# Kernel tuning notes

Hardware: AMD Instinct MI355X
Metric: run time of the kernel (lower is better)

Reference implementation:

```python
import jax, jax.numpy as jnp
import numpy as np

H = 8
D_MODEL = 1024
D_K = D_MODEL // H
NEG = -1000000000.0


def layer_norm(x, a, b, eps=1e-06):
    # torch std: unbiased (ddof=1); module divides by (std + eps)
    mean = jnp.mean(x, axis=-1, keepdims=True)
    var = jnp.sum((x - mean) ** 2, axis=-1, keepdims=True) / (x.shape[-1] - 1)
    std = jnp.sqrt(var)
    return a * (x - mean) / (std + eps) + b


def setup_inputs() -> dict:
    key = jax.random.key(0)
    ks = jax.random.split(key, 12)
    B, S, D = 8, 1024, D_MODEL
    inp = {
        "query": jax.random.normal(ks[0], (B, S, D), jnp.float32),
        "value": jax.random.normal(ks[1], (B, S, D), jnp.float32),
        "key": jax.random.normal(ks[2], (B, S, D), jnp.float32),
        "mask": jax.random.randint(ks[3], (B, S), 0, 2, jnp.int32),
        "ln_a": jnp.ones((D,), jnp.float32),
        "ln_b": jnp.zeros((D,), jnp.float32),
        "wq": jax.random.normal(ks[4], (D, D), jnp.float32) * 0.02,
        "bq": jnp.zeros((D,), jnp.float32),
        "wk": jax.random.normal(ks[5], (D, D), jnp.float32) * 0.02,
        "bk": jnp.zeros((D,), jnp.float32),
        "wv": jax.random.normal(ks[6], (D, D), jnp.float32) * 0.02,
        "bv": jnp.zeros((D,), jnp.float32),
        "w_aoa": jax.random.normal(ks[7], (2 * D, 2 * D), jnp.float32) * 0.02,  # [out, in]
        "b_aoa": jnp.zeros((2 * D,), jnp.float32),
    }
    return inp


def reference(query, value, key, mask, ln_a, ln_b, wq, bq, wk, bk, wv, bv, w_aoa, b_aoa):
    B, S, D = query.shape
    # mask [B,S] -> [B,1,1,S]
    m = mask[:, None, None, :]
    # norm_q
    q = layer_norm(query, ln_a, ln_b)
    # QKV projections, split heads -> [B,H,S,Dk]
    def split_heads(x):
        return x.reshape(B, -1, H, D_K).transpose(0, 2, 1, 3)
    q_ = split_heads(q @ wq.T + bq)
    k_ = split_heads(key @ wk.T + bk)
    v_ = split_heads(value @ wv.T + bv)
    scores = jnp.einsum("bhqd,bhkd->bhqk", q_, k_) / jnp.sqrt(jnp.float32(D_K))
    scores = jnp.where(m == 0, NEG, scores)
    p = jax.nn.softmax(scores, axis=-1)
    x = jnp.einsum("bhqk,bhkd->bhqd", p, v_)
    x = x.transpose(0, 2, 1, 3).reshape(B, S, D)
    # AoA: concat with (normed) query, linear to 2D, GLU
    z = jnp.concatenate([x, q], axis=-1) @ w_aoa.T + b_aoa
    a, g = jnp.split(z, 2, axis=-1)
    return a * jax.nn.sigmoid(g)
```

## Files before the change

### kernel.cpp

```cpp
#include <hip/hip_runtime.h>

typedef __attribute__((ext_vector_type(8))) __bf16 bf16x8;
typedef __attribute__((ext_vector_type(4))) float f32x4;
typedef __attribute__((ext_vector_type(16))) float f32x16;
typedef __attribute__((ext_vector_type(2))) int i32x2;

__device__ __forceinline__ ushort f2b(float f) {
    uint u = __builtin_bit_cast(uint, f);
    u += 0x7fffu + ((u >> 16) & 1u);
    return (ushort)(u >> 16);
}
__device__ __forceinline__ float b2f(ushort h) {
    uint u = ((uint)h) << 16;
    return __builtin_bit_cast(float, u);
}
__device__ __forceinline__ uint cvtpk(float a, float b) {
    uint r;
    asm("v_cvt_pk_bf16_f32 %0, %1, %2" : "=v"(r) : "v"(a), "v"(b));
    return r;
}

__global__ __launch_bounds__(256) void cast_all(const float* __restrict__ key,
                                                const float* __restrict__ value,
                                                const float* __restrict__ wq,
                                                const float* __restrict__ wk,
                                                const float* __restrict__ wv,
                                                const float* __restrict__ waoa,
                                                ushort* __restrict__ keyb,
                                                ushort* __restrict__ wqb,
                                                ushort* __restrict__ wab) {
    int bid = blockIdx.x;
    int tid = threadIdx.x;
    if (bid < 16384) {
        const float* src = (bid < 8192) ? key : value;
        float4 v = *(const float4*)(src + ((size_t)(bid & 8191) * 256 + tid) * 4);
        ushort4 o;
        o.x = f2b(v.x); o.y = f2b(v.y); o.z = f2b(v.z); o.w = f2b(v.w);
        *(ushort4*)(keyb + (size_t)bid * 1024 + tid * 4) = o;
    } else if (bid < 19456) {
        int b2 = bid - 16384;
        const float* src = (b2 < 1024) ? wq : ((b2 < 2048) ? wk : wv);
        float4 v = *(const float4*)(src + ((size_t)(b2 & 1023) * 256 + tid) * 4);
        ushort4 o;
        o.x = f2b(v.x); o.y = f2b(v.y); o.z = f2b(v.z); o.w = f2b(v.w);
        *(ushort4*)(wqb + (size_t)b2 * 1024 + tid * 4) = o;
    } else {
        int b3 = bid - 19456;
        int n1 = b3 >> 1;
        int c = (b3 & 1) * 1024 + tid * 4;
        int q = ((n1 & 63) | ((n1 >> 7) << 6)) + ((n1 >> 6) & 1) * 1024;
        float4 v = *(const float4*)(waoa + (size_t)q * 2048 + c);
        ushort4 o;
        o.x = f2b(v.x); o.y = f2b(v.y); o.z = f2b(v.z); o.w = f2b(v.w);
        *(ushort4*)(wab + (size_t)n1 * 2048 + c) = o;
    }
}

__global__ __launch_bounds__(256) void ln_kernel(const float* __restrict__ x,
                                                 const float* __restrict__ ga,
                                                 const float* __restrict__ be,
                                                 ushort* __restrict__ xq) {
    const int row = blockIdx.x, tid = threadIdx.x;
    __shared__ float red[4];
    float4 v = ((const float4*)(x + (size_t)row * 1024))[tid];
    float sm = v.x + v.y + v.z + v.w;
    for (int off = 32; off; off >>= 1) sm += __shfl_xor(sm, off);
    if ((tid & 63) == 0) red[tid >> 6] = sm;
    __syncthreads();
    float mean = (red[0] + red[1] + red[2] + red[3]) * (1.f / 1024.f);
    __syncthreads();
    float dx = v.x - mean, dy = v.y - mean, dz = v.z - mean, dw = v.w - mean;
    float s2 = dx * dx + dy * dy + dz * dz + dw * dw;
    for (int off = 32; off; off >>= 1) s2 += __shfl_xor(s2, off);
    if ((tid & 63) == 0) red[tid >> 6] = s2;
    __syncthreads();
    float var = (red[0] + red[1] + red[2] + red[3]) * (1.f / 1023.f);
    float inv = 1.f / (sqrtf(var) + 1e-6f);
    float4 g = ((const float4*)ga)[tid];
    float4 bb = ((const float4*)be)[tid];
    ushort4 o;
    o.x = f2b(g.x * dx * inv + bb.x);
    o.y = f2b(g.y * dy * inv + bb.y);
    o.z = f2b(g.z * dz * inv + bb.z);
    o.w = f2b(g.w * dw * inv + bb.w);
    *(ushort4*)&xq[(size_t)row * 2048 + 1024 + tid * 4] = o;
}

template <int MODE>
__global__ __launch_bounds__(512, 2) void gemm6(const ushort* __restrict__ Aq, int ldaq,
                                                const ushort* __restrict__ B, int ldb,
                                                const float* __restrict__ bias0,
                                                void* __restrict__ out0,
                                                int K, int NB) {
    __shared__ ushort lds[2][32768];

    const int tid = threadIdx.x;
    const int w = tid >> 6, l = tid & 63;
    const int wr = w >> 2, wcn = w & 3;
    const int r16 = l & 15, g4 = l >> 4;

    const int bid = blockIdx.x;
    const int cpx = gridDim.x >> 3;
    const int swz = (bid & 7) * cpx + (bid >> 3);
    const int m0 = (swz / NB) * 256;
    const int n0 = (swz % NB) * 256;

    const ushort* A = Aq;
    const int lda = ldaq;

    const int srow8 = l >> 3;
    const int sxor8 = ((l & 7) ^ srow8) * 8;
    const ushort* As0 = A + (size_t)(m0 + w * 8 + srow8) * lda + sxor8;
    const ushort* Bs0 = B + (size_t)(n0 + w * 8 + srow8) * ldb + sxor8;

    f32x4 acc[8][4];
#pragma unroll
    for (int i = 0; i < 8; i++)
#pragma unroll
        for (int j = 0; j < 4; j++) acc[i][j] = (f32x4){0.f, 0.f, 0.f, 0.f};

    const int sw16 = (r16 & 7) << 4;
    char* ldsb = (char*)&lds[0][0];

#define STAGE_H(sel_, HS_, kt_)                                                            \
    do {                                                                                   \
        const int mat_ = (HS_)&1, half_ = (HS_) >> 1;                                      \
        const ushort* sb_ = mat_ ? Bs0 : As0;                                              \
        const int ld_ = mat_ ? ldb : lda;                                                  \
        _Pragma("unroll") for (int li_ = 0; li_ < 2; li_++) {                              \
            const ushort* src_ = sb_ + (size_t)(half_ * 128 + li_ * 64) * ld_ + (kt_)*64;  \
            int dst_ = (sel_)*65536 + mat_ * 32768 + half_ * 16384 + li_ * 8192 + w * 1024;\
            __builtin_amdgcn_global_load_lds(                                              \
                (const __attribute__((address_space(1))) void*)src_,                       \
                (__attribute__((address_space(3))) void*)(ldsb + dst_), 16, 0, 0);         \
        }                                                                                  \
    } while (0)

    auto LDA4 = [&](bf16x8 (&dst)[4][2], int sel, int half) {
#pragma unroll
        for (int ai = 0; ai < 4; ai++)
#pragma unroll
            for (int ks = 0; ks < 2; ks++)
                dst[ai][ks] = *(const bf16x8*)(ldsb + sel * 65536 + half * 16384 +
                                               (wr * 16 + 32 * ai + r16) * 128 +
                                               ((ks * 64 + g4 * 16) ^ sw16));
    };
    auto LDB2 = [&](bf16x8 (&dst)[2][2], int sel, int half) {
#pragma unroll
        for (int bi = 0; bi < 2; bi++)
#pragma unroll
            for (int ks = 0; ks < 2; ks++)
                dst[bi][ks] = *(const bf16x8*)(ldsb + sel * 65536 + 32768 + half * 16384 +
                                               (wcn * 16 + 64 * bi + r16) * 128 +
                                               ((ks * 64 + g4 * 16) ^ sw16));
    };
    auto MM = [&](bf16x8 (&af)[4][2], bf16x8 (&bf)[2][2], int A0, int B0) {
        __builtin_amdgcn_s_setprio(1);
#pragma unroll
        for (int ks = 0; ks < 2; ks++)
#pragma unroll
            for (int ai = 0; ai < 4; ai++)
#pragma unroll
                for (int bi = 0; bi < 2; bi++)
                    acc[A0 + ai][B0 + bi] = __builtin_amdgcn_mfma_f32_16x16x32_bf16(
                        af[ai][ks], bf[bi][ks], acc[A0 + ai][B0 + bi], 0, 0, 0);
        __builtin_amdgcn_s_setprio(0);
    };

    const int NT = K >> 6;

    STAGE_H(0, 0, 0); STAGE_H(0, 1, 0); STAGE_H(0, 2, 0); STAGE_H(0, 3, 0);
    STAGE_H(1, 0, 1); STAGE_H(1, 1, 1); STAGE_H(1, 2, 1);
    asm volatile("s_waitcnt vmcnt(10)" ::: "memory");
    __builtin_amdgcn_s_barrier();

    bf16x8 aL[4][2], aH[4][2], bL[2][2], bH[2][2];

    for (int t = 0; t < NT - 2; ++t) {
        const int sel = t & 1;
        LDA4(aL, sel, 0); LDB2(bL, sel, 0);
        STAGE_H(sel ^ 1, 3, t + 1);
        __builtin_amdgcn_s_barrier();
        MM(aL, bL, 0, 0);
        asm volatile("s_waitcnt vmcnt(10)" ::: "memory");
        __builtin_amdgcn_s_barrier();
        LDA4(aH, sel, 1);
        STAGE_H(sel, 0, t + 2);
        __builtin_amdgcn_s_barrier();
        MM(aH, bL, 4, 0);
        asm volatile("s_waitcnt vmcnt(10)" ::: "memory");
        __builtin_amdgcn_s_barrier();
        LDB2(bH, sel, 1);
        STAGE_H(sel, 1, t + 2);
        __builtin_amdgcn_s_barrier();
        MM(aH, bH, 4, 2);
        __builtin_amdgcn_s_barrier();
        STAGE_H(sel, 2, t + 2);
        __builtin_amdgcn_s_barrier();
        MM(aL, bH, 0, 2);
        asm volatile("s_waitcnt vmcnt(10)" ::: "memory");
        __builtin_amdgcn_s_barrier();
    }
    {
        const int sel = (NT - 2) & 1;
        LDA4(aL, sel, 0); LDB2(bL, sel, 0);
        STAGE_H(sel ^ 1, 3, NT - 1);
        __builtin_amdgcn_s_barrier();
        MM(aL, bL, 0, 0);
        asm volatile("s_waitcnt vmcnt(10)" ::: "memory");
        __builtin_amdgcn_s_barrier();
        LDA4(aH, sel, 1);
        __builtin_amdgcn_s_barrier();
        MM(aH, bL, 4, 0);
        asm volatile("s_waitcnt vmcnt(8)" ::: "memory");
        __builtin_amdgcn_s_barrier();
        LDB2(bH, sel, 1);
        __builtin_amdgcn_s_barrier();
        MM(aH, bH, 4, 2);
        __builtin_amdgcn_s_barrier();
        MM(aL, bH, 0, 2);
        asm volatile("s_waitcnt vmcnt(4)" ::: "memory");
        __builtin_amdgcn_s_barrier();
    }
    {
        const int sel = (NT - 1) & 1;
        LDA4(aL, sel, 0); LDB2(bL, sel, 0);
        __builtin_amdgcn_s_barrier();
        MM(aL, bL, 0, 0);
        asm volatile("s_waitcnt vmcnt(2)" ::: "memory");
        __builtin_amdgcn_s_barrier();
        LDA4(aH, sel, 1);
        __builtin_amdgcn_s_barrier();
        MM(aH, bL, 4, 0);
        asm volatile("s_waitcnt vmcnt(0)" ::: "memory");
        __builtin_amdgcn_s_barrier();
        LDB2(bH, sel, 1);
        MM(aH, bH, 4, 2);
        MM(aL, bH, 0, 2);
    }
#undef STAGE_H

    float* out = (float*)out0;
#pragma unroll
    for (int bp = 0; bp < 2; bp++) {
        int j = (n0 >> 1) + wcn * 16 + 64 * bp + r16;
        float bsa = bias0[j];
        float bsg = bias0[j + 1024];
#pragma unroll
        for (int a_ = 0; a_ < 8; a_++) {
            int mr = m0 + wr * 16 + 32 * a_ + g4 * 4;
#pragma unroll
            for (int r = 0; r < 4; r++) {
                float av = acc[a_][2 * bp][r] + bsa;
                float gv = acc[a_][2 * bp + 1][r] + bsg;
                out[(size_t)(mr + r) * 1024 + j] = av * (1.f / (1.f + __expf(-gv)));
            }
        }
    }
}

__global__ __launch_bounds__(512, 2) void gemm7(const ushort* __restrict__ Aq, int ldaq,
                                                const ushort* __restrict__ Ak,
                                                const ushort* __restrict__ Av,
                                                const ushort* __restrict__ B, int ldb,
                                                const float* __restrict__ bias0,
                                                const float* __restrict__ bias1,
                                                const float* __restrict__ bias2,
                                                ushort* __restrict__ out0,
                                                ushort* __restrict__ out1,
                                                ushort* __restrict__ out2,
                                                float qscale) {
    __shared__ ushort lds[2][24576];

    const int tid = threadIdx.x;
    const int w = tid >> 6, l = tid & 63;
    const int wr = w >> 2, wcn = w & 3;
    const int r16 = l & 15, g4 = l >> 4;

    const int bid = blockIdx.x;
    const int cpx = gridDim.x >> 3;
    const int swz = (bid & 7) * cpx + (bid >> 3);
    const int m0 = (swz / 12) * 128;
    const int n0 = (swz % 12) * 256;

    const int region = n0 >> 10;
    const ushort* A = region == 0 ? Aq : (region == 1 ? Ak : Av);
    const int lda = region == 0 ? ldaq : 1024;

    const int srow8 = l >> 3;
    const int sxor8 = ((l & 7) ^ srow8) * 8;
    const ushort* As0 = A + (size_t)(m0 + w * 8 + srow8) * lda + sxor8;
    const ushort* Bs0 = B + (size_t)(n0 + w * 8 + srow8) * ldb + sxor8;

    f32x4 acc[4][4];
#pragma unroll
    for (int i = 0; i < 4; i++)
#pragma unroll
        for (int j = 0; j < 4; j++) acc[i][j] = (f32x4){0.f, 0.f, 0.f, 0.f};

    const int sw16 = (r16 & 7) << 4;
    char* ldsb = (char*)&lds[0][0];

#define STAGE_A(sel_, h_, kt_)                                                             \
    __builtin_amdgcn_global_load_lds(                                                      \
        (const __attribute__((address_space(1))) void*)(As0 + (size_t)((h_)*64) * lda + (kt_)*64), \
        (__attribute__((address_space(3))) void*)(ldsb + (sel_)*49152 + (h_)*8192 + w * 1024), 16, 0, 0)
#define STAGE_B(sel_, h_, li_, kt_)                                                        \
    __builtin_amdgcn_global_load_lds(                                                      \
        (const __attribute__((address_space(1))) void*)(Bs0 + (size_t)((h_)*128 + (li_)*64) * ldb + (kt_)*64), \
        (__attribute__((address_space(3))) void*)(ldsb + (sel_)*49152 + 16384 + (h_)*16384 + (li_)*8192 + w * 1024), 16, 0, 0)

    auto LDA2 = [&](bf16x8 (&dst)[2][2], int sel, int half) {
#pragma unroll
        for (int ai = 0; ai < 2; ai++)
#pragma unroll
            for (int ks = 0; ks < 2; ks++)
                dst[ai][ks] = *(const bf16x8*)(ldsb + sel * 49152 + half * 8192 +
                                               (wr * 16 + 32 * ai + r16) * 128 +
                                               ((ks * 64 + g4 * 16) ^ sw16));
    };
    auto LDB2 = [&](bf16x8 (&dst)[2][2], int sel, int half) {
#pragma unroll
        for (int bi = 0; bi < 2; bi++)
#pragma unroll
            for (int ks = 0; ks < 2; ks++)
                dst[bi][ks] = *(const bf16x8*)(ldsb + sel * 49152 + 16384 + half * 16384 +
                                               (wcn * 16 + 64 * bi + r16) * 128 +
                                               ((ks * 64 + g4 * 16) ^ sw16));
    };
    auto MM = [&](bf16x8 (&af)[2][2], bf16x8 (&bf)[2][2], int A0, int B0) {
        __builtin_amdgcn_s_setprio(1);
#pragma unroll
        for (int ks = 0; ks < 2; ks++)
#pragma unroll
            for (int ai = 0; ai < 2; ai++)
#pragma unroll
                for (int bi = 0; bi < 2; bi++)
                    acc[A0 + ai][B0 + bi] = __builtin_amdgcn_mfma_f32_16x16x32_bf16(
                        af[ai][ks], bf[bi][ks], acc[A0 + ai][B0 + bi], 0, 0, 0);
        __builtin_amdgcn_s_setprio(0);
    };

    const int NT = 16;

    STAGE_A(0, 0, 0); STAGE_B(0, 0, 0, 0); STAGE_B(0, 0, 1, 0);
    STAGE_A(0, 1, 0); STAGE_B(0, 1, 0, 0); STAGE_B(0, 1, 1, 0);
    STAGE_A(1, 0, 1); STAGE_B(1, 0, 0, 1); STAGE_B(1, 0, 1, 1);
    STAGE_A(1, 1, 1);
    asm volatile("s_waitcnt vmcnt(7)" ::: "memory");
    __builtin_amdgcn_s_barrier();

    bf16x8 aL[2][2], aH[2][2], bL[2][2], bH[2][2];

    for (int t = 0; t < NT - 2; ++t) {
        const int sel = t & 1;
        LDA2(aL, sel, 0); LDB2(bL, sel, 0);
        STAGE_B(sel ^ 1, 1, 0, t + 1); STAGE_B(sel ^ 1, 1, 1, t + 1);
        __builtin_amdgcn_s_barrier();
        MM(aL, bL, 0, 0);
        asm volatile("s_waitcnt vmcnt(8)" ::: "memory");
        __builtin_amdgcn_s_barrier();
        LDA2(aH, sel, 1);
        STAGE_A(sel, 0, t + 2);
        __builtin_amdgcn_s_barrier();
        MM(aH, bL, 2, 0);
        asm volatile("s_waitcnt vmcnt(7)" ::: "memory");
        __builtin_amdgcn_s_barrier();
        LDB2(bH, sel, 1);
        STAGE_B(sel, 0, 0, t + 2); STAGE_B(sel, 0, 1, t + 2);
        __builtin_amdgcn_s_barrier();
        MM(aH, bH, 2, 2);
        __builtin_amdgcn_s_barrier();
        STAGE_A(sel, 1, t + 2);
        __builtin_amdgcn_s_barrier();
        MM(aL, bH, 0, 2);
        asm volatile("s_waitcnt vmcnt(7)" ::: "memory");
        __builtin_amdgcn_s_barrier();
    }
    {
        const int sel = (NT - 2) & 1;
        LDA2(aL, sel, 0); LDB2(bL, sel, 0);
        STAGE_B(sel ^ 1, 1, 0, NT - 1); STAGE_B(sel ^ 1, 1, 1, NT - 1);
        __builtin_amdgcn_s_barrier();
        MM(aL, bL, 0, 0);
        asm volatile("s_waitcnt vmcnt(8)" ::: "memory");
        __builtin_amdgcn_s_barrier();
        LDA2(aH, sel, 1);
        __builtin_amdgcn_s_barrier();
        MM(aH, bL, 2, 0);
        asm volatile("s_waitcnt vmcnt(6)" ::: "memory");
        __builtin_amdgcn_s_barrier();
        LDB2(bH, sel, 1);
        __builtin_amdgcn_s_barrier();
        MM(aH, bH, 2, 2);
        __builtin_amdgcn_s_barrier();
        MM(aL, bH, 0, 2);
        asm volatile("s_waitcnt vmcnt(3)" ::: "memory");
        __builtin_amdgcn_s_barrier();
    }
    {
        const int sel = (NT - 1) & 1;
        LDA2(aL, sel, 0); LDB2(bL, sel, 0);
        __builtin_amdgcn_s_barrier();
        MM(aL, bL, 0, 0);
        asm volatile("s_waitcnt vmcnt(2)" ::: "memory");
        __builtin_amdgcn_s_barrier();
        LDA2(aH, sel, 1);
        __builtin_amdgcn_s_barrier();
        MM(aH, bL, 2, 0);
        asm volatile("s_waitcnt vmcnt(0)" ::: "memory");
        __builtin_amdgcn_s_barrier();
        LDB2(bH, sel, 1);
        MM(aH, bH, 2, 2);
        MM(aL, bH, 0, 2);
    }
#undef STAGE_A
#undef STAGE_B

    const int nr0 = n0 & 1023;
    const float* bias = region == 0 ? bias0 : (region == 1 ? bias1 : bias2);
    const float scale = region == 0 ? qscale : 1.f;
    if (region < 2) {
        ushort* C = region == 0 ? out0 : out1;
#pragma unroll
        for (int b_ = 0; b_ < 4; b_++) {
            int n = nr0 + wcn * 16 + 64 * b_ + r16;
            float bs = bias[n];
#pragma unroll
            for (int a_ = 0; a_ < 4; a_++) {
                int mr = m0 + wr * 16 + 32 * a_ + g4 * 4;
#pragma unroll
                for (int r = 0; r < 4; r++)
                    C[(size_t)(mr + r) * 1024 + n] = f2b((acc[a_][b_][r] + bs) * scale);
            }
        }
    } else {
        ushort* Vt = out2;
#pragma unroll
        for (int b_ = 0; b_ < 4; b_++) {
            int n = nr0 + wcn * 16 + 64 * b_ + r16;
            float bs = bias[n];
            int h = n >> 7, d = n & 127;
#pragma unroll
            for (int a_ = 0; a_ < 4; a_++) {
                int mr = m0 + wr * 16 + 32 * a_ + g4 * 4;
                int bb = mr >> 10, s_ = mr & 1023;
                ushort4 o;
                o.x = f2b(acc[a_][b_][0] + bs);
                o.y = f2b(acc[a_][b_][1] + bs);
                o.z = f2b(acc[a_][b_][2] + bs);
                o.w = f2b(acc[a_][b_][3] + bs);
                *(ushort4*)&Vt[((size_t)(bb * 8 + h) * 128 + d) * 1024 + s_] = o;
            }
        }
    }
}

__global__ __launch_bounds__(256, 2) void attn_kernel(const ushort* __restrict__ Q,
                                                      const ushort* __restrict__ Kt,
                                                      const ushort* __restrict__ Vt,
                                                      const int* __restrict__ mask,
                                                      ushort* __restrict__ xq) {
    __shared__ ushort Ks[2][8192];
    __shared__ ushort Vs[2][8192];

    const int tid = threadIdx.x;
    const int l = tid & 63, wid = tid >> 6;
    const int ql = l & 31, hi = l >> 5;
    const int id = blockIdx.x;
    const int bh = ((id >> 6) << 3) | (id & 7);
    const int qb = (id >> 3) & 7;
    const int b = bh >> 3, h = bh & 7;
    const int q0 = qb * 128 + wid * 32;

    bf16x8 qf[8];
    const ushort* Qrow = Q + (size_t)(b * 1024 + q0 + ql) * 1024 + h * 128 + hi * 8;
#pragma unroll
    for (int ks = 0; ks < 8; ks++) qf[ks] = *(const bf16x8*)(Qrow + ks * 16);

    const ushort* Kg = Kt + ((size_t)b * 1024) * 1024 + h * 128;
    const ushort* Vg = Vt + (size_t)(b * 8 + h) * 128 * 1024;
    const int* mptr = mask + b * 1024;

    f32x16 xacc[4];
#pragma unroll
    for (int i = 0; i < 4; i++)
#pragma unroll
        for (int r = 0; r < 16; r++) xacc[i][r] = 0.f;
    float mrow = -INFINITY, lrow = 0.f, sclp = 0.f;
    bool resc = true;
    bf16x8 pa[4];

    auto STAGE_K = [&](int sel, int t) {
        const int kv0 = t * 64;
#pragma unroll
        for (int it = 0; it < 4; ++it) {
            int ob = it * 4096 + wid * 1024;
            int o = ob + l * 16;
            int row = o >> 8;
            int sc = (o & 255) ^ ((row & 7) << 4);
            const ushort* src = Kg + (size_t)(kv0 + row) * 1024 + (sc >> 1);
            __builtin_amdgcn_global_load_lds((const __attribute__((address_space(1))) void*)src,
                (__attribute__((address_space(3))) void*)((char*)&Ks[sel][0] + ob), 16, 0, 0);
        }
    };
    auto STAGE_V = [&](int sel, int t) {
        const int kv0 = t * 64;
#pragma unroll
        for (int it = 0; it < 4; ++it) {
            int ob = it * 4096 + wid * 1024;
            int o = ob + l * 16;
            int d = o >> 7;
            int sc = (o & 127) ^ ((d & 7) << 4);
            const ushort* src = Vg + (size_t)d * 1024 + kv0 + (sc >> 1);
            __builtin_amdgcn_global_load_lds((const __attribute__((address_space(1))) void*)src,
                (__attribute__((address_space(3))) void*)((char*)&Vs[sel][0] + ob), 16, 0, 0);
        }
    };

    auto QK = [&](f32x16 (&s)[2], int sel, unsigned long long wt) {
        const char* Kb_ = (const char*)&Ks[sel][0];
#pragma unroll
        for (int sub = 0; sub < 2; sub++) {
            f32x16 sa, sb;
#pragma unroll
            for (int r = 0; r < 16; r++) { sa[r] = 0.f; sb[r] = 0.f; }
            const int rowk = sub * 32 + ql;
            const char* kr = Kb_ + rowk * 256;
            const int sw = (rowk & 7) << 4;
            __builtin_amdgcn_s_setprio(1);
#pragma unroll
            for (int ks = 0; ks < 4; ks++) {
                bf16x8 k0 = *(const bf16x8*)(kr + (((2 * ks) * 32 + hi * 16) ^ sw));
                bf16x8 k1 = *(const bf16x8*)(kr + (((2 * ks + 1) * 32 + hi * 16) ^ sw));
                sa = __builtin_amdgcn_mfma_f32_32x32x16_bf16(k0, qf[2 * ks], sa, 0, 0, 0);
                sb = __builtin_amdgcn_mfma_f32_32x32x16_bf16(k1, qf[2 * ks + 1], sb, 0, 0, 0);
            }
            __builtin_amdgcn_s_setprio(0);
#pragma unroll
            for (int r = 0; r < 16; r++) sa[r] += sb[r];
#pragma unroll
            for (int q2 = 0; q2 < 4; q2++) {
                uint nib = (uint)(wt >> (8 * q2 + 4 * hi + 32 * sub)) & 15u;
#pragma unroll
                for (int r = 0; r < 4; r++)
                    if (!((nib >> r) & 1u)) sa[4 * q2 + r] = -1e9f;
            }
            s[sub] = sa;
        }
    };
    auto PV = [&](int sel) {
        const char* Vb_ = (const char*)&Vs[sel][0];
        if (resc) {
#pragma unroll
            for (int df = 0; df < 4; df++)
#pragma unroll
                for (int r = 0; r < 16; r++) xacc[df][r] *= sclp;
        }
        __builtin_amdgcn_s_setprio(1);
#pragma unroll
        for (int ks2 = 0; ks2 < 4; ks2++) {
#pragma unroll
            for (int df = 0; df < 4; df++) {
                const int d = df * 32 + ql;
                bf16x8 vfr = *(const bf16x8*)(Vb_ + d * 128 + ((ks2 * 32 + hi * 16) ^ ((d & 7) << 4)));
                xacc[df] = __builtin_amdgcn_mfma_f32_32x32x16_bf16(vfr, pa[ks2], xacc[df], 0, 0, 0);
            }
        }
        __builtin_amdgcn_s_setprio(0);
    };
    auto SOFTMAX = [&](f32x16 (&s)[2]) {
        float v[16];
#pragma unroll
        for (int r = 0; r < 16; r++) v[r] = fmaxf(s[0][r], s[1][r]);
#pragma unroll
        for (int st = 8; st; st >>= 1)
#pragma unroll
            for (int i = 0; i < 8; i++)
                if (i < st) v[i] = fmaxf(v[i], v[i + st]);
        float pmax = fmaxf(v[0], __shfl_xor(v[0], 32));
        if (!__all(pmax - mrow <= 8.f)) {
            float mn = fmaxf(mrow, pmax);
            sclp = __expf(mrow - mn);
            mrow = mn;
            resc = true;
        } else {
            resc = false;
        }
        float rsum = 0.f;
#pragma unroll
        for (int res = 0; res < 2; res++)
#pragma unroll
            for (int r = 0; r < 16; r++) {
                float p = __expf(s[res][r] - mrow);
                s[res][r] = p;
                rsum += p;
            }
        rsum += __shfl_xor(rsum, 32);
        lrow = (resc ? lrow * sclp : lrow) + rsum;
#pragma unroll
        for (int sub = 0; sub < 2; sub++)
#pragma unroll
            for (int g = 0; g < 2; g++) {
                const int b0 = g * 8;
                uint lo01 = cvtpk(s[sub][b0 + 0], s[sub][b0 + 1]);
                uint lo23 = cvtpk(s[sub][b0 + 2], s[sub][b0 + 3]);
                uint hi01 = cvtpk(s[sub][b0 + 4], s[sub][b0 + 5]);
                uint hi23 = cvtpk(s[sub][b0 + 6], s[sub][b0 + 7]);
                i32x2 r02 = __builtin_amdgcn_permlane32_swap((int)lo01, (int)hi01, false, false);
                i32x2 r13 = __builtin_amdgcn_permlane32_swap((int)lo23, (int)hi23, false, false);
                union { bf16x8 vv; uint u[4]; } pk;
                pk.u[0] = (uint)r02.x;
                pk.u[1] = (uint)r13.x;
                pk.u[2] = (uint)r02.y;
                pk.u[3] = (uint)r13.y;
                pa[sub * 2 + g] = pk.vv;
            }
    };

    STAGE_K(0, 0);
    int mv = mptr[l];
    asm volatile("s_waitcnt vmcnt(0)" ::: "memory");
    __syncthreads();
    STAGE_K(1, 1);
    STAGE_V(0, 0);
    unsigned long long wt = __ballot(mv != 0);
    mv = mptr[64 + l];
    f32x16 s[2];
    QK(s, 0, wt);
    SOFTMAX(s);
    int kc = 1, vc = 0;

    for (int u = 1; u < 16; ++u) {
        wt = __ballot(mv != 0);
        asm volatile("s_waitcnt vmcnt(0)" ::: "memory");
        __syncthreads();
        if (u < 15) STAGE_K(kc ^ 1, u + 1);
        STAGE_V(vc ^ 1, u);
        if (u < 15) mv = mptr[(u + 1) * 64 + l];

        QK(s, kc, wt);
        PV(vc);
        SOFTMAX(s);

        kc ^= 1; vc ^= 1;
    }

    asm volatile("s_waitcnt vmcnt(0)" ::: "memory");
    __syncthreads();
    PV(vc);

    const float inv = 1.f / lrow;
    const size_t orow = (size_t)(b * 1024 + q0 + ql) * 2048 + h * 128;
#pragma unroll
    for (int df = 0; df < 4; df++) {
#pragma unroll
        for (int q2 = 0; q2 < 4; q2++) {
            ushort4 o;
            o.x = f2b(xacc[df][4 * q2 + 0] * inv);
            o.y = f2b(xacc[df][4 * q2 + 1] * inv);
            o.z = f2b(xacc[df][4 * q2 + 2] * inv);
            o.w = f2b(xacc[df][4 * q2 + 3] * inv);
            *(ushort4*)&xq[orow + df * 32 + 8 * q2 + 4 * hi] = o;
        }
    }
}

extern "C" void kernel_launch(void* const* d_in, const int* in_sizes, int n_in,
                              void* d_out, int out_size, void* d_ws, size_t ws_size,
                              hipStream_t stream) {
    const float* query = (const float*)d_in[0];
    const float* value = (const float*)d_in[1];
    const float* key   = (const float*)d_in[2];
    const int*   mask  = (const int*)d_in[3];
    const float* ln_a  = (const float*)d_in[4];
    const float* ln_b  = (const float*)d_in[5];
    const float* wq    = (const float*)d_in[6];
    const float* bq    = (const float*)d_in[7];
    const float* wk    = (const float*)d_in[8];
    const float* bk    = (const float*)d_in[9];
    const float* wv    = (const float*)d_in[10];
    const float* bv    = (const float*)d_in[11];
    const float* waoa  = (const float*)d_in[12];
    const float* baoa  = (const float*)d_in[13];
    float* out = (float*)d_out;

    char* w8 = (char*)d_ws;
    ushort* xq   = (ushort*)(w8);
    ushort* Qb   = (ushort*)(w8 + 33554432);
    ushort* Kb   = (ushort*)(w8 + 50331648);
    ushort* Vt   = (ushort*)(w8 + 67108864);
    ushort* keyb = (ushort*)(w8 + 83886080);
    ushort* wqb  = (ushort*)(w8 + 117440512);
    ushort* wab  = (ushort*)(w8 + 123731968);

    cast_all<<<23552, 256, 0, stream>>>(key, value, wq, wk, wv, waoa, keyb, wqb, wab);
    ln_kernel<<<8192, 256, 0, stream>>>(query, ln_a, ln_b, xq);

    const float qscale = 0.08838834764831845f;
    ushort* valb = keyb + 8388608;

    gemm7<<<768, 512, 0, stream>>>(xq + 1024, 2048, keyb, valb,
                                   wqb, 1024, bq, bk, bv,
                                   Qb, Kb, Vt, qscale);

    attn_kernel<<<512, 256, 0, stream>>>(Qb, Kb, Vt, mask, xq);

    gemm6<1><<<256, 512, 0, stream>>>(xq, 2048, wab, 2048, baoa, out, 2048, 8);
}
```

Baseline: 229.1 us.

## Fuse fp32-to-bf16 cast of key/value into K/V projection GEMM

Result: faster. 216.2 us, median of 4 (-5.7%).

```diff
diff --git a/kernel.cpp b/kernel.cpp
--- a/kernel.cpp
+++ b/kernel.cpp
@@ -20,32 +20,22 @@
     return r;
 }
 
-__global__ __launch_bounds__(256) void cast_all(const float* __restrict__ key,
-                                                const float* __restrict__ value,
-                                                const float* __restrict__ wq,
+__global__ __launch_bounds__(256) void cast_all(const float* __restrict__ wq,
                                                 const float* __restrict__ wk,
                                                 const float* __restrict__ wv,
                                                 const float* __restrict__ waoa,
-                                                ushort* __restrict__ keyb,
                                                 ushort* __restrict__ wqb,
                                                 ushort* __restrict__ wab) {
     int bid = blockIdx.x;
     int tid = threadIdx.x;
-    if (bid < 16384) {
-        const float* src = (bid < 8192) ? key : value;
-        float4 v = *(const float4*)(src + ((size_t)(bid & 8191) * 256 + tid) * 4);
+    if (bid < 3072) {
+        const float* src = (bid < 1024) ? wq : ((bid < 2048) ? wk : wv);
+        float4 v = *(const float4*)(src + ((size_t)(bid & 1023) * 256 + tid) * 4);
         ushort4 o;
         o.x = f2b(v.x); o.y = f2b(v.y); o.z = f2b(v.z); o.w = f2b(v.w);
-        *(ushort4*)(keyb + (size_t)bid * 1024 + tid * 4) = o;
-    } else if (bid < 19456) {
-        int b2 = bid - 16384;
-        const float* src = (b2 < 1024) ? wq : ((b2 < 2048) ? wk : wv);
-        float4 v = *(const float4*)(src + ((size_t)(b2 & 1023) * 256 + tid) * 4);
-        ushort4 o;
-        o.x = f2b(v.x); o.y = f2b(v.y); o.z = f2b(v.z); o.w = f2b(v.w);
-        *(ushort4*)(wqb + (size_t)b2 * 1024 + tid * 4) = o;
+        *(ushort4*)(wqb + (size_t)bid * 1024 + tid * 4) = o;
     } else {
-        int b3 = bid - 19456;
+        int b3 = bid - 3072;
         int n1 = b3 >> 1;
         int c = (b3 & 1) * 1024 + tid * 4;
         int q = ((n1 & 63) | ((n1 >> 7) << 6)) + ((n1 >> 6) & 1) * 1024;
@@ -259,17 +249,10 @@
     }
 }
 
-__global__ __launch_bounds__(512, 2) void gemm7(const ushort* __restrict__ Aq, int ldaq,
-                                                const ushort* __restrict__ Ak,
-                                                const ushort* __restrict__ Av,
-                                                const ushort* __restrict__ B, int ldb,
-                                                const float* __restrict__ bias0,
-                                                const float* __restrict__ bias1,
-                                                const float* __restrict__ bias2,
-                                                ushort* __restrict__ out0,
-                                                ushort* __restrict__ out1,
-                                                ushort* __restrict__ out2,
-                                                float qscale) {
+__global__ __launch_bounds__(512, 2) void gemm7q(const ushort* __restrict__ A, int lda,
+                                                 const ushort* __restrict__ B, int ldb,
+                                                 const float* __restrict__ bias,
+                                                 ushort* __restrict__ C, float qscale) {
     __shared__ ushort lds[2][24576];
 
     const int tid = threadIdx.x;
@@ -280,12 +263,8 @@
     const int bid = blockIdx.x;
     const int cpx = gridDim.x >> 3;
     const int swz = (bid & 7) * cpx + (bid >> 3);
-    const int m0 = (swz / 12) * 128;
-    const int n0 = (swz % 12) * 256;
-
-    const int region = n0 >> 10;
-    const ushort* A = region == 0 ? Aq : (region == 1 ? Ak : Av);
-    const int lda = region == 0 ? ldaq : 1024;
+    const int m0 = (swz >> 2) * 128;
+    const int n0 = (swz & 3) * 256;
 
     const int srow8 = l >> 3;
     const int sxor8 = ((l & 7) ^ srow8) * 8;
@@ -417,11 +396,171 @@
 #undef STAGE_A
 #undef STAGE_B
 
+#pragma unroll
+    for (int b_ = 0; b_ < 4; b_++) {
+        int n = n0 + wcn * 16 + 64 * b_ + r16;
+        float bs = bias[n];
+#pragma unroll
+        for (int a_ = 0; a_ < 4; a_++) {
+            int mr = m0 + wr * 16 + 32 * a_ + g4 * 4;
+#pragma unroll
+            for (int r = 0; r < 4; r++)
+                C[(size_t)(mr + r) * 1024 + n] = f2b((acc[a_][b_][r] + bs) * qscale);
+        }
+    }
+}
+
+__global__ __launch_bounds__(512, 2) void gemm7kv(const float* __restrict__ Akf,
+                                                  const float* __restrict__ Avf,
+                                                  const ushort* __restrict__ B, int ldb,
+                                                  const float* __restrict__ biask,
+                                                  const float* __restrict__ biasv,
+                                                  ushort* __restrict__ Kb,
+                                                  ushort* __restrict__ Vt) {
+    __shared__ ushort lds[2][24576];
+
+    const int tid = threadIdx.x;
+    const int w = tid >> 6, l = tid & 63;
+    const int wr = w >> 2, wcn = w & 3;
+    const int r16 = l & 15, g4 = l >> 4;
+
+    const int bid = blockIdx.x;
+    const int cpx = gridDim.x >> 3;
+    const int swz = (bid & 7) * cpx + (bid >> 3);
+    const int m0 = (swz >> 3) * 128;
+    const int n0 = (swz & 7) * 256;
+    const int kreg = n0 >> 10;
+    const float* Af = kreg ? Avf : Akf;
+
+    const int srow8 = l >> 3;
+    const int sxor8 = ((l & 7) ^ srow8) * 8;
+    const ushort* Bs0 = B + (size_t)(n0 + w * 8 + srow8) * ldb + sxor8;
+
+    const int arow = w * 8 + srow8;
+    const float* As0 = Af + (size_t)(m0 + arow) * 1024 + (l & 7) * 8;
+    const int awr = arow * 128 + (((l & 7) * 16) ^ ((arow & 7) << 4));
+
+    f32x4 acc[4][4];
+#pragma unroll
+    for (int i = 0; i < 4; i++)
+#pragma unroll
+        for (int j = 0; j < 4; j++) acc[i][j] = (f32x4){0.f, 0.f, 0.f, 0.f};
+
+    const int sw16 = (r16 & 7) << 4;
+    char* ldsb = (char*)&lds[0][0];
+
+#define STAGE_B(sel_, h_, li_, kt_)                                                        \
+    __builtin_amdgcn_global_load_lds(                                                      \
+        (const __attribute__((address_space(1))) void*)(Bs0 + (size_t)((h_)*128 + (li_)*64) * ldb + (kt_)*64), \
+        (__attribute__((address_space(3))) void*)(ldsb + (sel_)*49152 + 16384 + (h_)*16384 + (li_)*8192 + w * 1024), 16, 0, 0)
+
+    float4 ah[2][2];
+    auto GL4 = [&](float4& d, const float* p) {
+        asm volatile("global_load_dwordx4 %0, %1, off" : "=&v"(d) : "v"(p) : "memory");
+    };
+    auto LOAD_A = [&](int kt) {
+#pragma unroll
+        for (int h = 0; h < 2; h++) {
+            const float* p = As0 + (size_t)h * 64 * 1024 + kt * 64;
+            GL4(ah[h][0], p);
+            GL4(ah[h][1], p + 4);
+        }
+    };
+    auto WRITE_A = [&](int sel) {
+#pragma unroll
+        for (int h = 0; h < 2; h++) {
+            union { bf16x8 v; uint u[4]; } pk;
+            pk.u[0] = cvtpk(ah[h][0].x, ah[h][0].y);
+            pk.u[1] = cvtpk(ah[h][0].z, ah[h][0].w);
+            pk.u[2] = cvtpk(ah[h][1].x, ah[h][1].y);
+            pk.u[3] = cvtpk(ah[h][1].z, ah[h][1].w);
+            *(bf16x8*)(ldsb + sel * 49152 + h * 8192 + awr) = pk.v;
+        }
+    };
+
+    auto LDA2 = [&](bf16x8 (&dst)[2][2], int sel, int half) {
+#pragma unroll
+        for (int ai = 0; ai < 2; ai++)
+#pragma unroll
+            for (int ks = 0; ks < 2; ks++)
+                dst[ai][ks] = *(const bf16x8*)(ldsb + sel * 49152 + half * 8192 +
+                                               (wr * 16 + 32 * ai + r16) * 128 +
+                                               ((ks * 64 + g4 * 16) ^ sw16));
+    };
+    auto LDB2 = [&](bf16x8 (&dst)[2][2], int sel, int half) {
+#pragma unroll
+        for (int bi = 0; bi < 2; bi++)
+#pragma unroll
+            for (int ks = 0; ks < 2; ks++)
+                dst[bi][ks] = *(const bf16x8*)(ldsb + sel * 49152 + 16384 + half * 16384 +
+                                               (wcn * 16 + 64 * bi + r16) * 128 +
+                                               ((ks * 64 + g4 * 16) ^ sw16));
+    };
+    auto MM = [&](bf16x8 (&af)[2][2], bf16x8 (&bf)[2][2], int A0, int B0) {
+        __builtin_amdgcn_s_setprio(1);
+#pragma unroll
+        for (int ks = 0; ks < 2; ks++)
+#pragma unroll
+            for (int ai = 0; ai < 2; ai++)
+#pragma unroll
+                for (int bi = 0; bi < 2; bi++)
+                    acc[A0 + ai][B0 + bi] = __builtin_amdgcn_mfma_f32_16x16x32_bf16(
+                        af[ai][ks], bf[bi][ks], acc[A0 + ai][B0 + bi], 0, 0, 0);
+        __builtin_amdgcn_s_setprio(0);
+    };
+
+    const int NT = 16;
+
+    STAGE_B(0, 0, 0, 0); STAGE_B(0, 0, 1, 0);
+    LOAD_A(0);
+    STAGE_B(0, 1, 0, 0); STAGE_B(0, 1, 1, 0);
+    asm volatile("s_waitcnt vmcnt(2)" ::: "memory");
+    __builtin_amdgcn_sched_barrier(0);
+    WRITE_A(0);
+    asm volatile("s_waitcnt lgkmcnt(0)" ::: "memory");
+    __builtin_amdgcn_sched_barrier(0);
+    __builtin_amdgcn_s_barrier();
+
+    bf16x8 aL[2][2], aH[2][2], bL[2][2], bH[2][2];
+
+    for (int t = 0; t < NT; ++t) {
+        const int sel = t & 1;
+        const bool pf = (t + 1 < NT);
+        LDA2(aL, sel, 0); LDB2(bL, sel, 0);
+        if (pf) {
+            STAGE_B(sel ^ 1, 0, 0, t + 1); STAGE_B(sel ^ 1, 0, 1, t + 1);
+            LOAD_A(t + 1);
+        }
+        __builtin_amdgcn_s_barrier();
+        MM(aL, bL, 0, 0);
+        __builtin_amdgcn_s_barrier();
+        LDA2(aH, sel, 1);
+        __builtin_amdgcn_s_barrier();
+        MM(aH, bL, 2, 0);
+        if (pf) asm volatile("s_waitcnt vmcnt(6)" ::: "memory");
+        else    asm volatile("s_waitcnt vmcnt(0)" ::: "memory");
+        __builtin_amdgcn_s_barrier();
+        LDB2(bH, sel, 1);
+        if (pf) { STAGE_B(sel ^ 1, 1, 0, t + 1); STAGE_B(sel ^ 1, 1, 1, t + 1); }
+        __builtin_amdgcn_s_barrier();
+        MM(aH, bH, 2, 2);
+        __builtin_amdgcn_s_barrier();
+        if (pf) {
+            asm volatile("s_waitcnt vmcnt(2)" ::: "memory");
+            __builtin_amdgcn_sched_barrier(0);
+            WRITE_A(sel ^ 1);
+            asm volatile("s_waitcnt lgkmcnt(0)" ::: "memory");
+            __builtin_amdgcn_sched_barrier(0);
+        }
+        __builtin_amdgcn_s_barrier();
+        MM(aL, bH, 0, 2);
+        __builtin_amdgcn_s_barrier();
+    }
+#undef STAGE_B
+
     const int nr0 = n0 & 1023;
-    const float* bias = region == 0 ? bias0 : (region == 1 ? bias1 : bias2);
-    const float scale = region == 0 ? qscale : 1.f;
-    if (region < 2) {
-        ushort* C = region == 0 ? out0 : out1;
+    const float* bias = kreg ? biasv : biask;
+    if (kreg == 0) {
 #pragma unroll
         for (int b_ = 0; b_ < 4; b_++) {
             int n = nr0 + wcn * 16 + 64 * b_ + r16;
@@ -431,11 +570,10 @@
                 int mr = m0 + wr * 16 + 32 * a_ + g4 * 4;
 #pragma unroll
                 for (int r = 0; r < 4; r++)
-                    C[(size_t)(mr + r) * 1024 + n] = f2b((acc[a_][b_][r] + bs) * scale);
+                    Kb[(size_t)(mr + r) * 1024 + n] = f2b(acc[a_][b_][r] + bs);
             }
         }
     } else {
-        ushort* Vt = out2;
 #pragma unroll
         for (int b_ = 0; b_ < 4; b_++) {
             int n = nr0 + wcn * 16 + 64 * b_ + r16;
@@ -690,19 +828,16 @@
     ushort* Qb   = (ushort*)(w8 + 33554432);
     ushort* Kb   = (ushort*)(w8 + 50331648);
     ushort* Vt   = (ushort*)(w8 + 67108864);
-    ushort* keyb = (ushort*)(w8 + 83886080);
     ushort* wqb  = (ushort*)(w8 + 117440512);
     ushort* wab  = (ushort*)(w8 + 123731968);
 
-    cast_all<<<23552, 256, 0, stream>>>(key, value, wq, wk, wv, waoa, keyb, wqb, wab);
+    cast_all<<<7168, 256, 0, stream>>>(wq, wk, wv, waoa, wqb, wab);
     ln_kernel<<<8192, 256, 0, stream>>>(query, ln_a, ln_b, xq);
 
     const float qscale = 0.08838834764831845f;
-    ushort* valb = keyb + 8388608;
-
-    gemm7<<<768, 512, 0, stream>>>(xq + 1024, 2048, keyb, valb,
-                                   wqb, 1024, bq, bk, bv,
-                                   Qb, Kb, Vt, qscale);
+
+    gemm7q<<<256, 512, 0, stream>>>(xq + 1024, 2048, wqb, 1024, bq, Qb, qscale);
+    gemm7kv<<<512, 512, 0, stream>>>(key, value, wqb + 1048576, 1024, bk, bv, Kb, Vt);
 
     attn_kernel<<<512, 256, 0, stream>>>(Qb, Kb, Vt, mask, xq);
 
```
